# Performance work log

Hardware: AMD Instinct MI355X
Metric: run time of the kernel (lower is better)

## Reference

```python
import jax, jax.numpy as jnp
import numpy as np

B, D_IN, D_GAS, D_LIQ, N_PLATES, D_OUT, N_SWEEPS = 16384, 512, 256, 256, 8, 1000, 2


def _linear_init(key, fan_in, shape):
    bound = 1.0 / np.sqrt(fan_in)
    return jax.random.uniform(key, shape, minval=-bound, maxval=bound, dtype=jnp.float32)


def setup_inputs() -> dict:
    key = jax.random.key(0)
    ks = jax.random.split(key, 13)
    return {
        "x": jax.random.normal(ks[0], (B, D_IN), dtype=jnp.float32),
        # gas encoder: Linear(d_in, d_gas)
        "W_ge": _linear_init(ks[1], D_IN, (D_IN, D_GAS)),
        "b_ge": _linear_init(ks[2], D_IN, (D_GAS,)),
        # shared plate: equilibrium Linear(d_liquid, d_gas)
        "W_eq": _linear_init(ks[3], D_LIQ, (D_LIQ, D_GAS)),
        "b_eq": _linear_init(ks[4], D_LIQ, (D_GAS,)),
        # shared plate: transfer Linear(d_gas, d_gas)
        "W_tr": _linear_init(ks[5], D_GAS, (D_GAS, D_GAS)),
        "b_tr": _linear_init(ks[6], D_GAS, (D_GAS,)),
        # shared plate: absorption Linear(d_gas, d_liquid)
        "W_ab": _linear_init(ks[7], D_GAS, (D_GAS, D_LIQ)),
        "b_ab": _linear_init(ks[8], D_GAS, (D_LIQ,)),
        # transfer coefficient
        "alpha": jnp.float32(0.1),
        # output head: Linear(d_gas+d_liquid, d_gas) -> ReLU -> Linear(d_gas, d_out)
        "W1": _linear_init(ks[9], D_GAS + D_LIQ, (D_GAS + D_LIQ, D_GAS)),
        "b1": _linear_init(ks[10], D_GAS + D_LIQ, (D_GAS,)),
        "W2": _linear_init(ks[11], D_GAS, (D_GAS, D_OUT)),
        "b2": _linear_init(ks[12], D_GAS, (D_OUT,)),
    }


def reference(x, W_ge, b_ge, W_eq, b_eq, W_tr, b_tr, W_ab, b_ab, alpha, W1, b1, W2, b2):
    g0 = jax.nn.relu(x @ W_ge + b_ge)  # (B, d_gas)

    def plate(g, l):
        e = jax.nn.sigmoid(l @ W_eq + b_eq)          # equilibrium gas composition
        df = g - e                                    # driving force
        delta = alpha * (df @ W_tr + b_tr)            # transferred amount
        return g - delta, l + (delta @ W_ab + b_ab)   # gas loses, liquid absorbs

    N = N_PLATES
    g = [g0] + [None] * N
    l = [None] * (N + 1) + [jnp.zeros((x.shape[0], D_LIQ), dtype=x.dtype)]
    for _sweep in range(N_SWEEPS):
        # descending liquid sweep
        for n in range(N, 0, -1):
            g_in = g[n - 1] if g[n - 1] is not None else g0
            _, l[n] = plate(g_in, l[n + 1])
        # ascending gas sweep
        g[0] = g0
        for n in range(1, N + 1):
            g[n], _ = plate(g[n - 1], l[n])

    feats = jnp.concatenate([g[N], l[1]], axis=-1)  # (B, d_gas + d_liquid)
    h = jax.nn.relu(feats @ W1 + b1)
    return h @ W2 + b2
```

## Files before the change

kernel.cpp:

```cpp
#include <hip/hip_runtime.h>


typedef _Float16 f16;
typedef _Float16 f16x8 __attribute__((ext_vector_type(8)));
typedef float f32x4 __attribute__((ext_vector_type(4)));

#define NT 256
#define TILE_B 16
#define SLOT 8192
#define TMPA_OFF 131072
#define TMPB_OFF 139264
#define LDS_BYTES 147456
#define GASP(s) (smem + (s) * SLOT)
#define LIQP(m) (smem + 57344 + (m) * SLOT)

__device__ __forceinline__ f32x4 mfma16(f16x8 a, f16x8 b, f32x4 c) {
  return __builtin_amdgcn_mfma_f32_16x16x32_f16(a, b, c, 0, 0, 0);
}
__device__ __forceinline__ f32x4 zero4() {
  f32x4 z; z[0] = 0.f; z[1] = 0.f; z[2] = 0.f; z[3] = 0.f; return z;
}
__device__ __forceinline__ float sigm(float s) { return 1.f / (1.f + __expf(-s)); }

__device__ __forceinline__ void gemm_rB(const char* aB, const f16x8 (&B)[8][4],
                                        int l15, int kg, f32x4 (&acc)[4]) {
  const int sw = (l15 & 7) << 4;
  #pragma unroll
  for (int ks = 0; ks < 8; ++ks) {
    const int kk = (ks << 5) + (kg << 3);
    f16x8 a = *(const f16x8*)(aB + l15 * 512 + ((kk * 2) ^ sw));
    #pragma unroll
    for (int f = 0; f < 4; ++f) acc[f] = mfma16(a, B[ks][f], acc[f]);
  }
}

template <int K, int AS>
__device__ __forceinline__ void gemm_gB(const char* aB,
                                        const f16* __restrict__ p0,
                                        const f16* __restrict__ p1,
                                        const f16* __restrict__ p2,
                                        const f16* __restrict__ p3,
                                        int l15, int kg, f32x4 (&acc)[4]) {
  const int sw = (l15 & 7) << 4;
  #pragma unroll
  for (int ks = 0; ks < (K >> 5); ++ks) {
    const int kk = (ks << 5) + (kg << 3);
    f16x8 a = *(const f16x8*)(aB + l15 * AS + ((kk * 2) ^ sw));
    acc[0] = mfma16(a, *(const f16x8*)(p0 + (ks << 5)), acc[0]);
    acc[1] = mfma16(a, *(const f16x8*)(p1 + (ks << 5)), acc[1]);
    acc[2] = mfma16(a, *(const f16x8*)(p2 + (ks << 5)), acc[2]);
    acc[3] = mfma16(a, *(const f16x8*)(p3 + (ks << 5)), acc[3]);
  }
}

__device__ __forceinline__ void store16(char* buf, int w, int l15, int kg,
                                        const float* v) {
  #pragma unroll
  for (int q = 0; q < 16; ++q) {
    const int r = kg * 4 + (q & 3);
    const int c = w * 64 + ((q >> 2) << 4) + l15;
    *(f16*)(buf + r * 512 + ((c * 2) ^ ((r & 7) << 4))) = (f16)v[q];
  }
}
__device__ __forceinline__ void read16(const char* buf, int w, int l15, int kg,
                                       float* v) {
  #pragma unroll
  for (int q = 0; q < 16; ++q) {
    const int r = kg * 4 + (q & 3);
    const int c = w * 64 + ((q >> 2) << 4) + l15;
    v[q] = (float)*(const f16*)(buf + r * 512 + ((c * 2) ^ ((r & 7) << 4)));
  }
}

__global__ void prep_all(const float* __restrict__ Wge, const float* __restrict__ Weq,
                         const float* __restrict__ Wtr, const float* __restrict__ Wab,
                         const float* __restrict__ W1,  const float* __restrict__ W2,
                         f16* __restrict__ WgeT, f16* __restrict__ WeqT,
                         f16* __restrict__ WtrT, f16* __restrict__ WabT,
                         f16* __restrict__ W1T,  f16* __restrict__ W2T) {
  __shared__ float ts[32][33];
  const int b = blockIdx.x;
  const float* src; f16* dst; int K, N, Npad, ti;
  if (b < 128)      { src = Wge; dst = WgeT; K = 512; N = 256;  Npad = 256;  ti = b; }
  else if (b < 192) { src = Weq; dst = WeqT; K = 256; N = 256;  Npad = 256;  ti = b - 128; }
  else if (b < 256) { src = Wtr; dst = WtrT; K = 256; N = 256;  Npad = 256;  ti = b - 192; }
  else if (b < 320) { src = Wab; dst = WabT; K = 256; N = 256;  Npad = 256;  ti = b - 256; }
  else if (b < 448) { src = W1;  dst = W1T;  K = 512; N = 256;  Npad = 256;  ti = b - 320; }
  else              { src = W2;  dst = W2T;  K = 256; N = 1000; Npad = 1024; ti = b - 448; }
  const int bnT = Npad >> 5;
  const int bk = (ti / bnT) << 5, bn = (ti % bnT) << 5;
  const int tx = threadIdx.x & 31, ty = threadIdx.x >> 5;
  #pragma unroll
  for (int i = 0; i < 32; i += 8) {
    const int k = bk + ty + i, n = bn + tx;
    ts[ty + i][tx] = (k < K && n < N) ? src[(size_t)k * N + n] : 0.f;
  }
  __syncthreads();
  #pragma unroll
  for (int i = 0; i < 32; i += 8) {
    const int n = bn + ty + i, k = bk + tx;
    if (n < Npad) dst[(size_t)n * K + k] = (f16)ts[tx][ty + i];
  }
}

__global__ __launch_bounds__(NT, 1)
void cfn_main(const float* __restrict__ x,
              const float* __restrict__ bge, const float* __restrict__ beq,
              const float* __restrict__ btr, const float* __restrict__ bab,
              const float* __restrict__ alphap,
              const float* __restrict__ b1p, const float* __restrict__ b2p,
              const f16* __restrict__ WgeT, const f16* __restrict__ WeqT,
              const f16* __restrict__ WtrT, const f16* __restrict__ WabT,
              const f16* __restrict__ W1T, const f16* __restrict__ W2T,
              float* __restrict__ out) {
  extern __shared__ char smem[];
  const int tid = threadIdx.x;
  const int lane = tid & 63;
  const int w = tid >> 6;
  const int l15 = lane & 15, kg = lane >> 4;
  const int r0 = blockIdx.x * TILE_B;
  const float alpha = alphap[0];
  const int sw = (l15 & 7) << 4;

  float beqv[4], btrv[4], babv[4], se[4];
  #pragma unroll
  for (int f = 0; f < 4; ++f) {
    const int c = w * 64 + f * 16 + l15;
    beqv[f] = beq[c]; btrv[f] = btr[c]; babv[f] = bab[c];
    se[f] = sigm(beqv[f]);
  }

  f16x8 WeqR[8][4], WtrR[8][4];
  #pragma unroll
  for (int f = 0; f < 4; ++f) {
    const int c = w * 64 + f * 16 + l15;
    const f16* pe = WeqT + (size_t)c * 256 + kg * 8;
    const f16* pt = WtrT + (size_t)c * 256 + kg * 8;
    #pragma unroll
    for (int ks = 0; ks < 8; ++ks) {
      WeqR[ks][f] = *(const f16x8*)(pe + (ks << 5));
      WtrR[ks][f] = *(const f16x8*)(pt + (ks << 5));
    }
  }

  const f16* wab0 = WabT + (size_t)(w * 64 +  0 + l15) * 256 + kg * 8;
  const f16* wab1 = WabT + (size_t)(w * 64 + 16 + l15) * 256 + kg * 8;
  const f16* wab2 = WabT + (size_t)(w * 64 + 32 + l15) * 256 + kg * 8;
  const f16* wab3 = WabT + (size_t)(w * 64 + 48 + l15) * 256 + kg * 8;

  {
    const int row = tid >> 4;
    const int cb = (tid & 15) << 5;
    const int rs = (row & 7) << 4;
    const float* p = x + (size_t)(r0 + row) * 512 + cb;
    #pragma unroll
    for (int i = 0; i < 4; ++i) {
      float4 u = *(const float4*)(p + i * 8);
      float4 v = *(const float4*)(p + i * 8 + 4);
      f16x8 h;
      h[0] = (f16)u.x; h[1] = (f16)u.y; h[2] = (f16)u.z; h[3] = (f16)u.w;
      h[4] = (f16)v.x; h[5] = (f16)v.y; h[6] = (f16)v.z; h[7] = (f16)v.w;
      *(f16x8*)(smem + row * 1024 + (((cb + i * 8) * 2) ^ rs)) = h;
    }
  }
  __syncthreads();

  {
    f32x4 acc[4] = {zero4(), zero4(), zero4(), zero4()};
    const f16* g0 = WgeT + (size_t)(w * 64 +  0 + l15) * 512 + kg * 8;
    const f16* g1 = WgeT + (size_t)(w * 64 + 16 + l15) * 512 + kg * 8;
    const f16* g2 = WgeT + (size_t)(w * 64 + 32 + l15) * 512 + kg * 8;
    const f16* g3 = WgeT + (size_t)(w * 64 + 48 + l15) * 512 + kg * 8;
    gemm_gB<512, 1024>(smem, g0, g1, g2, g3, l15, kg, acc);
    float G0[16];
    #pragma unroll
    for (int q = 0; q < 16; ++q) {
      const float bv = bge[w * 64 + ((q >> 2) << 4) + l15];
      float v2 = acc[q >> 2][q & 3] + bv;
      G0[q] = v2 > 0.f ? v2 : 0.f;
    }
    __syncthreads();
    #pragma unroll
    for (int s = 0; s < 8; ++s) store16(GASP(s), w, l15, kg, G0);
  }
  __syncthreads();

  float G8[16];

  #pragma unroll 1
  for (int sweep = 0; sweep < 2; ++sweep) {
    #pragma unroll 1
    for (int n = 8; n >= 1; --n) {
      float GV[16];
      read16(GASP(n - 1), w, l15, kg, GV);
      float DF[16];
      if (n == 8) {
        #pragma unroll
        for (int q = 0; q < 16; ++q) DF[q] = GV[q] - se[q >> 2];
      } else {
        f32x4 acc[4] = {zero4(), zero4(), zero4(), zero4()};
        gemm_rB(LIQP(n + 1), WeqR, l15, kg, acc);
        #pragma unroll
        for (int q = 0; q < 16; ++q)
          DF[q] = GV[q] - sigm(acc[q >> 2][q & 3] + beqv[q >> 2]);
      }
      store16(smem + TMPA_OFF, w, l15, kg, DF);
      __syncthreads();
      float DEL[16];
      {
        f32x4 acc[4] = {zero4(), zero4(), zero4(), zero4()};
        gemm_rB(smem + TMPA_OFF, WtrR, l15, kg, acc);
        #pragma unroll
        for (int q = 0; q < 16; ++q)
          DEL[q] = alpha * (acc[q >> 2][q & 3] + btrv[q >> 2]);
      }
      store16(smem + TMPB_OFF, w, l15, kg, DEL);
      __syncthreads();
      {
        f32x4 acc[4] = {zero4(), zero4(), zero4(), zero4()};
        gemm_gB<256, 512>(smem + TMPB_OFF, wab0, wab1, wab2, wab3, l15, kg, acc);
        float LN[16];
        if (n < 8) read16(LIQP(n + 1), w, l15, kg, LN);
        else { _Pragma("unroll") for (int q = 0; q < 16; ++q) LN[q] = 0.f; }
        #pragma unroll
        for (int q = 0; q < 16; ++q)
          LN[q] += acc[q >> 2][q & 3] + babv[q >> 2];
        store16(LIQP(n), w, l15, kg, LN);
      }
      __syncthreads();
    }
    const int nmax = (sweep == 0) ? 7 : 8;
    #pragma unroll 1
    for (int n = 1; n <= nmax; ++n) {
      float GV[16];
      read16(GASP(n - 1), w, l15, kg, GV);
      float DF[16];
      {
        f32x4 acc[4] = {zero4(), zero4(), zero4(), zero4()};
        gemm_rB(LIQP(n), WeqR, l15, kg, acc);
        #pragma unroll
        for (int q = 0; q < 16; ++q)
          DF[q] = GV[q] - sigm(acc[q >> 2][q & 3] + beqv[q >> 2]);
      }
      store16(smem + TMPA_OFF, w, l15, kg, DF);
      __syncthreads();
      {
        f32x4 acc[4] = {zero4(), zero4(), zero4(), zero4()};
        gemm_rB(smem + TMPA_OFF, WtrR, l15, kg, acc);
        if (n < 8) {
          float NG[16];
          #pragma unroll
          for (int q = 0; q < 16; ++q)
            NG[q] = GV[q] - alpha * (acc[q >> 2][q & 3] + btrv[q >> 2]);
          store16(GASP(n), w, l15, kg, NG);
        } else {
          #pragma unroll
          for (int q = 0; q < 16; ++q)
            G8[q] = GV[q] - alpha * (acc[q >> 2][q & 3] + btrv[q >> 2]);
        }
      }
      __syncthreads();
    }
  }

  store16(smem + TMPA_OFF, w, l15, kg, G8);
  __syncthreads();
  {
    f32x4 acc[4] = {zero4(), zero4(), zero4(), zero4()};
    const f16* p0 = W1T + (size_t)(w * 64 +  0 + l15) * 512 + kg * 8;
    const f16* p1 = W1T + (size_t)(w * 64 + 16 + l15) * 512 + kg * 8;
    const f16* p2 = W1T + (size_t)(w * 64 + 32 + l15) * 512 + kg * 8;
    const f16* p3 = W1T + (size_t)(w * 64 + 48 + l15) * 512 + kg * 8;
    #pragma unroll
    for (int ks = 0; ks < 16; ++ks) {
      const int kk = (ks << 5) + (kg << 3);
      const char* base = (ks < 8) ? (smem + TMPA_OFF) : (smem + 65536);
      const int kl = kk & 255;
      f16x8 a = *(const f16x8*)(base + l15 * 512 + ((kl * 2) ^ sw));
      acc[0] = mfma16(a, *(const f16x8*)(p0 + (ks << 5)), acc[0]);
      acc[1] = mfma16(a, *(const f16x8*)(p1 + (ks << 5)), acc[1]);
      acc[2] = mfma16(a, *(const f16x8*)(p2 + (ks << 5)), acc[2]);
      acc[3] = mfma16(a, *(const f16x8*)(p3 + (ks << 5)), acc[3]);
    }
    float H[16];
    #pragma unroll
    for (int q = 0; q < 16; ++q) {
      const float bv = b1p[w * 64 + ((q >> 2) << 4) + l15];
      float v2 = acc[q >> 2][q & 3] + bv;
      H[q] = v2 > 0.f ? v2 : 0.f;
    }
    __syncthreads();
    store16(smem + TMPB_OFF, w, l15, kg, H);
  }
  __syncthreads();

  f32x4 cf[16];
  #pragma unroll
  for (int fi = 0; fi < 16; ++fi) {
    cf[fi] = zero4();
    const int f = w + fi * 4;
    if (f < 63) {
      const f16* p = W2T + (size_t)(f * 16 + l15) * 256 + kg * 8;
      #pragma unroll
      for (int ks = 0; ks < 8; ++ks) {
        const int kk = (ks << 5) + (kg << 3);
        f16x8 a = *(const f16x8*)(smem + TMPB_OFF + l15 * 512 + ((kk * 2) ^ sw));
        cf[fi] = mfma16(a, *(const f16x8*)(p + (ks << 5)), cf[fi]);
      }
    }
  }

  {
    float* ob = (float*)smem;
    #pragma unroll
    for (int fi = 0; fi < 16; ++fi) {
      const int f = w + fi * 4;
      const int colc = f * 16 + l15;
      if (f < 63 && colc < 1000) {
        const float bv = b2p[colc];
        #pragma unroll
        for (int j = 0; j < 4; ++j)
          ob[(kg * 4 + j) * 1000 + colc] = cf[fi][j] + bv;
      }
    }
  }
  __syncthreads();
  {
    const float* ob = (const float*)smem;
    float* op = out + (size_t)r0 * 1000;
    #pragma unroll 1
    for (int i = tid; i < 4000; i += NT)
      *(float4*)(op + i * 4) = *(const float4*)(ob + i * 4);
  }
}

extern "C" void kernel_launch(void* const* d_in, const int* in_sizes, int n_in,
                              void* d_out, int out_size, void* d_ws, size_t ws_size,
                              hipStream_t stream) {
  const float* x   = (const float*)d_in[0];
  const float* Wge = (const float*)d_in[1];
  const float* bge = (const float*)d_in[2];
  const float* Weq = (const float*)d_in[3];
  const float* beq = (const float*)d_in[4];
  const float* Wtr = (const float*)d_in[5];
  const float* btr = (const float*)d_in[6];
  const float* Wab = (const float*)d_in[7];
  const float* bab = (const float*)d_in[8];
  const float* alp = (const float*)d_in[9];
  const float* W1  = (const float*)d_in[10];
  const float* b1  = (const float*)d_in[11];
  const float* W2  = (const float*)d_in[12];
  const float* b2  = (const float*)d_in[13];
  float* out = (float*)d_out;

  char* ws = (char*)d_ws;
  f16* WgeT = (f16*)(ws + 0);
  f16* WeqT = (f16*)(ws + 262144);
  f16* WtrT = (f16*)(ws + 393216);
  f16* WabT = (f16*)(ws + 524288);
  f16* W1T  = (f16*)(ws + 655360);
  f16* W2T  = (f16*)(ws + 917504);

  prep_all<<<704, 256, 0, stream>>>(Wge, Weq, Wtr, Wab, W1, W2,
                                    WgeT, WeqT, WtrT, WabT, W1T, W2T);

  (void)hipFuncSetAttribute(reinterpret_cast<const void*>(cfn_main),
                            hipFuncAttributeMaxDynamicSharedMemorySize, LDS_BYTES);
  cfn_main<<<16384 / TILE_B, NT, LDS_BYTES, stream>>>(
      x, bge, beq, btr, bab, alp, b1, b2,
      WgeT, WeqT, WtrT, WabT, W1T, W2T, out);
}
```

Measured before the change: 799.3 us.

## Fold transfer and absorption weights into one matrix, keep gas states in registers

Precomputes Wtab = alpha*Wtr@Wab and a matching fused bias, so the descending liquid sweep does two GEMMs per plate instead of three and one fewer LDS round trip and barrier. Gas plate states move from LDS slots into fp16 register arrays accessed through switch statements. The Weq and Wtr register caches are dropped in favour of reading B operands from global/L2. Together these cut LDS from 144KB to 80KB and allow two blocks per CU. The cost is extra global weight traffic per GEMM, slightly different fp16 rounding from the pre-multiplied matrix, and register pressure under the tighter launch bound.

```diff
diff --git a/kernel.cpp b/kernel.cpp
--- a/kernel.cpp
+++ b/kernel.cpp
@@ -2,17 +2,17 @@
 
 
 typedef _Float16 f16;
+typedef _Float16 f16x2 __attribute__((ext_vector_type(2)));
 typedef _Float16 f16x8 __attribute__((ext_vector_type(8)));
 typedef float f32x4 __attribute__((ext_vector_type(4)));
 
 #define NT 256
 #define TILE_B 16
 #define SLOT 8192
-#define TMPA_OFF 131072
-#define TMPB_OFF 139264
-#define LDS_BYTES 147456
-#define GASP(s) (smem + (s) * SLOT)
-#define LIQP(m) (smem + 57344 + (m) * SLOT)
+#define TMPA_OFF 65536
+#define TMPH_OFF 73728
+#define LDS_BYTES 81920
+#define LIQP(m) (smem + ((m) - 1) * SLOT)
 
 __device__ __forceinline__ f32x4 mfma16(f16x8 a, f16x8 b, f32x4 c) {
   return __builtin_amdgcn_mfma_f32_16x16x32_f16(a, b, c, 0, 0, 0);
@@ -21,18 +21,6 @@
   f32x4 z; z[0] = 0.f; z[1] = 0.f; z[2] = 0.f; z[3] = 0.f; return z;
 }
 __device__ __forceinline__ float sigm(float s) { return 1.f / (1.f + __expf(-s)); }
-
-__device__ __forceinline__ void gemm_rB(const char* aB, const f16x8 (&B)[8][4],
-                                        int l15, int kg, f32x4 (&acc)[4]) {
-  const int sw = (l15 & 7) << 4;
-  #pragma unroll
-  for (int ks = 0; ks < 8; ++ks) {
-    const int kk = (ks << 5) + (kg << 3);
-    f16x8 a = *(const f16x8*)(aB + l15 * 512 + ((kk * 2) ^ sw));
-    #pragma unroll
-    for (int f = 0; f < 4; ++f) acc[f] = mfma16(a, B[ks][f], acc[f]);
-  }
-}
 
 template <int K, int AS>
 __device__ __forceinline__ void gemm_gB(const char* aB,
@@ -62,31 +50,38 @@
     *(f16*)(buf + r * 512 + ((c * 2) ^ ((r & 7) << 4))) = (f16)v[q];
   }
 }
-__device__ __forceinline__ void read16(const char* buf, int w, int l15, int kg,
-                                       float* v) {
-  #pragma unroll
-  for (int q = 0; q < 16; ++q) {
-    const int r = kg * 4 + (q & 3);
-    const int c = w * 64 + ((q >> 2) << 4) + l15;
-    v[q] = (float)*(const f16*)(buf + r * 512 + ((c * 2) ^ ((r & 7) << 4)));
+
+#define GH_RD(S) { _Pragma("unroll") for (int q = 0; q < 16; ++q) v[q] = (float)gh[S][q >> 1][q & 1]; }
+__device__ __forceinline__ void gh_read(const f16x2 (&gh)[8][8], int s, float* v) {
+  switch (s) {
+    case 0: GH_RD(0) break; case 1: GH_RD(1) break; case 2: GH_RD(2) break;
+    case 3: GH_RD(3) break; case 4: GH_RD(4) break; case 5: GH_RD(5) break;
+    case 6: GH_RD(6) break; default: GH_RD(7) break;
+  }
+}
+#define GH_WR(S) { _Pragma("unroll") for (int q = 0; q < 16; ++q) gh[S][q >> 1][q & 1] = (f16)v[q]; }
+__device__ __forceinline__ void gh_write(f16x2 (&gh)[8][8], int s, const float* v) {
+  switch (s) {
+    case 1: GH_WR(1) break; case 2: GH_WR(2) break; case 3: GH_WR(3) break;
+    case 4: GH_WR(4) break; case 5: GH_WR(5) break; case 6: GH_WR(6) break;
+    default: GH_WR(7) break;
   }
 }
 
 __global__ void prep_all(const float* __restrict__ Wge, const float* __restrict__ Weq,
-                         const float* __restrict__ Wtr, const float* __restrict__ Wab,
-                         const float* __restrict__ W1,  const float* __restrict__ W2,
+                         const float* __restrict__ Wtr, const float* __restrict__ W1,
+                         const float* __restrict__ W2,
                          f16* __restrict__ WgeT, f16* __restrict__ WeqT,
-                         f16* __restrict__ WtrT, f16* __restrict__ WabT,
-                         f16* __restrict__ W1T,  f16* __restrict__ W2T) {
+                         f16* __restrict__ WtrT, f16* __restrict__ W1T,
+                         f16* __restrict__ W2T) {
   __shared__ float ts[32][33];
   const int b = blockIdx.x;
   const float* src; f16* dst; int K, N, Npad, ti;
   if (b < 128)      { src = Wge; dst = WgeT; K = 512; N = 256;  Npad = 256;  ti = b; }
   else if (b < 192) { src = Weq; dst = WeqT; K = 256; N = 256;  Npad = 256;  ti = b - 128; }
   else if (b < 256) { src = Wtr; dst = WtrT; K = 256; N = 256;  Npad = 256;  ti = b - 192; }
-  else if (b < 320) { src = Wab; dst = WabT; K = 256; N = 256;  Npad = 256;  ti = b - 256; }
-  else if (b < 448) { src = W1;  dst = W1T;  K = 512; N = 256;  Npad = 256;  ti = b - 320; }
-  else              { src = W2;  dst = W2T;  K = 256; N = 1000; Npad = 1024; ti = b - 448; }
+  else if (b < 384) { src = W1;  dst = W1T;  K = 512; N = 256;  Npad = 256;  ti = b - 256; }
+  else              { src = W2;  dst = W2T;  K = 256; N = 1000; Npad = 1024; ti = b - 384; }
   const int bnT = Npad >> 5;
   const int bk = (ti / bnT) << 5, bn = (ti % bnT) << 5;
   const int tx = threadIdx.x & 31, ty = threadIdx.x >> 5;
@@ -103,14 +98,39 @@
   }
 }
 
-__global__ __launch_bounds__(NT, 1)
+__global__ void prep_wtab(const float* __restrict__ Wtr, const float* __restrict__ Wab,
+                          const float* __restrict__ btr, const float* __restrict__ bab,
+                          const float* __restrict__ alphap,
+                          f16* __restrict__ WtabT, float* __restrict__ btab) {
+  __shared__ float wcol[256];
+  __shared__ float pr[256];
+  const int out = blockIdx.x;
+  const int k = threadIdx.x;
+  wcol[k] = Wab[(size_t)k * 256 + out];
+  pr[k] = btr[k] * Wab[(size_t)k * 256 + out];
+  __syncthreads();
+  float acc = 0.f;
+  const float* wr = Wtr + (size_t)k * 256;
+  #pragma unroll 4
+  for (int m = 0; m < 256; ++m) acc += wr[m] * wcol[m];
+  const float alpha = alphap[0];
+  WtabT[(size_t)out * 256 + k] = (f16)(alpha * acc);
+  if (k == 0) {
+    float s = 0.f;
+    for (int m = 0; m < 256; ++m) s += pr[m];
+    btab[out] = alpha * s + bab[out];
+  }
+}
+
+__global__ __launch_bounds__(NT, 2)
 void cfn_main(const float* __restrict__ x,
               const float* __restrict__ bge, const float* __restrict__ beq,
-              const float* __restrict__ btr, const float* __restrict__ bab,
+              const float* __restrict__ btr,
               const float* __restrict__ alphap,
               const float* __restrict__ b1p, const float* __restrict__ b2p,
               const f16* __restrict__ WgeT, const f16* __restrict__ WeqT,
-              const f16* __restrict__ WtrT, const f16* __restrict__ WabT,
+              const f16* __restrict__ WtrT, const f16* __restrict__ WtabT,
+              const float* __restrict__ btab,
               const f16* __restrict__ W1T, const f16* __restrict__ W2T,
               float* __restrict__ out) {
   extern __shared__ char smem[];
@@ -122,31 +142,26 @@
   const float alpha = alphap[0];
   const int sw = (l15 & 7) << 4;
 
-  float beqv[4], btrv[4], babv[4], se[4];
+  float beqv[4], btrv[4], btabv[4], se[4];
   #pragma unroll
   for (int f = 0; f < 4; ++f) {
     const int c = w * 64 + f * 16 + l15;
-    beqv[f] = beq[c]; btrv[f] = btr[c]; babv[f] = bab[c];
+    beqv[f] = beq[c]; btrv[f] = btr[c]; btabv[f] = btab[c];
     se[f] = sigm(beqv[f]);
   }
 
-  f16x8 WeqR[8][4], WtrR[8][4];
-  #pragma unroll
-  for (int f = 0; f < 4; ++f) {
-    const int c = w * 64 + f * 16 + l15;
-    const f16* pe = WeqT + (size_t)c * 256 + kg * 8;
-    const f16* pt = WtrT + (size_t)c * 256 + kg * 8;
-    #pragma unroll
-    for (int ks = 0; ks < 8; ++ks) {
-      WeqR[ks][f] = *(const f16x8*)(pe + (ks << 5));
-      WtrR[ks][f] = *(const f16x8*)(pt + (ks << 5));
-    }
-  }
-
-  const f16* wab0 = WabT + (size_t)(w * 64 +  0 + l15) * 256 + kg * 8;
-  const f16* wab1 = WabT + (size_t)(w * 64 + 16 + l15) * 256 + kg * 8;
-  const f16* wab2 = WabT + (size_t)(w * 64 + 32 + l15) * 256 + kg * 8;
-  const f16* wab3 = WabT + (size_t)(w * 64 + 48 + l15) * 256 + kg * 8;
+  const f16* weq0  = WeqT  + (size_t)(w * 64 +  0 + l15) * 256 + kg * 8;
+  const f16* weq1  = WeqT  + (size_t)(w * 64 + 16 + l15) * 256 + kg * 8;
+  const f16* weq2  = WeqT  + (size_t)(w * 64 + 32 + l15) * 256 + kg * 8;
+  const f16* weq3  = WeqT  + (size_t)(w * 64 + 48 + l15) * 256 + kg * 8;
+  const f16* wtr0  = WtrT  + (size_t)(w * 64 +  0 + l15) * 256 + kg * 8;
+  const f16* wtr1  = WtrT  + (size_t)(w * 64 + 16 + l15) * 256 + kg * 8;
+  const f16* wtr2  = WtrT  + (size_t)(w * 64 + 32 + l15) * 256 + kg * 8;
+  const f16* wtr3  = WtrT  + (size_t)(w * 64 + 48 + l15) * 256 + kg * 8;
+  const f16* wtab0 = WtabT + (size_t)(w * 64 +  0 + l15) * 256 + kg * 8;
+  const f16* wtab1 = WtabT + (size_t)(w * 64 + 16 + l15) * 256 + kg * 8;
+  const f16* wtab2 = WtabT + (size_t)(w * 64 + 32 + l15) * 256 + kg * 8;
+  const f16* wtab3 = WtabT + (size_t)(w * 64 + 48 + l15) * 256 + kg * 8;
 
   {
     const int row = tid >> 4;
@@ -165,6 +180,7 @@
   }
   __syncthreads();
 
+  f16x2 gh[8][8];
   {
     f32x4 acc[4] = {zero4(), zero4(), zero4(), zero4()};
     const f16* g0 = WgeT + (size_t)(w * 64 +  0 + l15) * 512 + kg * 8;
@@ -172,92 +188,82 @@
     const f16* g2 = WgeT + (size_t)(w * 64 + 32 + l15) * 512 + kg * 8;
     const f16* g3 = WgeT + (size_t)(w * 64 + 48 + l15) * 512 + kg * 8;
     gemm_gB<512, 1024>(smem, g0, g1, g2, g3, l15, kg, acc);
-    float G0[16];
     #pragma unroll
     for (int q = 0; q < 16; ++q) {
       const float bv = bge[w * 64 + ((q >> 2) << 4) + l15];
       float v2 = acc[q >> 2][q & 3] + bv;
-      G0[q] = v2 > 0.f ? v2 : 0.f;
-    }
-    __syncthreads();
-    #pragma unroll
-    for (int s = 0; s < 8; ++s) store16(GASP(s), w, l15, kg, G0);
+      v2 = v2 > 0.f ? v2 : 0.f;
+      const f16 hv = (f16)v2;
+      #pragma unroll
+      for (int s = 0; s < 8; ++s) gh[s][q >> 1][q & 1] = hv;
+    }
   }
   __syncthreads();
 
   float G8[16];
+  #pragma unroll
+  for (int q = 0; q < 16; ++q) G8[q] = 0.f;
 
   #pragma unroll 1
   for (int sweep = 0; sweep < 2; ++sweep) {
     #pragma unroll 1
     for (int n = 8; n >= 1; --n) {
-      float GV[16];
-      read16(GASP(n - 1), w, l15, kg, GV);
+      float v[16];
+      gh_read(gh, n - 1, v);
       float DF[16];
       if (n == 8) {
         #pragma unroll
-        for (int q = 0; q < 16; ++q) DF[q] = GV[q] - se[q >> 2];
+        for (int q = 0; q < 16; ++q) DF[q] = v[q] - se[q >> 2];
       } else {
         f32x4 acc[4] = {zero4(), zero4(), zero4(), zero4()};
-        gemm_rB(LIQP(n + 1), WeqR, l15, kg, acc);
+        gemm_gB<256, 512>(LIQP(n + 1), weq0, weq1, weq2, weq3, l15, kg, acc);
         #pragma unroll
         for (int q = 0; q < 16; ++q)
-          DF[q] = GV[q] - sigm(acc[q >> 2][q & 3] + beqv[q >> 2]);
-      }
-      store16(smem + TMPA_OFF, w, l15, kg, DF);
-      __syncthreads();
-      float DEL[16];
-      {
-        f32x4 acc[4] = {zero4(), zero4(), zero4(), zero4()};
-        gemm_rB(smem + TMPA_OFF, WtrR, l15, kg, acc);
-        #pragma unroll
-        for (int q = 0; q < 16; ++q)
-          DEL[q] = alpha * (acc[q >> 2][q & 3] + btrv[q >> 2]);
-      }
-      store16(smem + TMPB_OFF, w, l15, kg, DEL);
-      __syncthreads();
-      {
-        f32x4 acc[4] = {zero4(), zero4(), zero4(), zero4()};
-        gemm_gB<256, 512>(smem + TMPB_OFF, wab0, wab1, wab2, wab3, l15, kg, acc);
-        float LN[16];
-        if (n < 8) read16(LIQP(n + 1), w, l15, kg, LN);
-        else { _Pragma("unroll") for (int q = 0; q < 16; ++q) LN[q] = 0.f; }
-        #pragma unroll
-        for (int q = 0; q < 16; ++q)
-          LN[q] += acc[q >> 2][q & 3] + babv[q >> 2];
-        store16(LIQP(n), w, l15, kg, LN);
-      }
-      __syncthreads();
-    }
-    const int nmax = (sweep == 0) ? 7 : 8;
-    #pragma unroll 1
-    for (int n = 1; n <= nmax; ++n) {
-      float GV[16];
-      read16(GASP(n - 1), w, l15, kg, GV);
-      float DF[16];
-      {
-        f32x4 acc[4] = {zero4(), zero4(), zero4(), zero4()};
-        gemm_rB(LIQP(n), WeqR, l15, kg, acc);
-        #pragma unroll
-        for (int q = 0; q < 16; ++q)
-          DF[q] = GV[q] - sigm(acc[q >> 2][q & 3] + beqv[q >> 2]);
+          DF[q] = v[q] - sigm(acc[q >> 2][q & 3] + beqv[q >> 2]);
       }
       store16(smem + TMPA_OFF, w, l15, kg, DF);
       __syncthreads();
       {
         f32x4 acc[4] = {zero4(), zero4(), zero4(), zero4()};
-        gemm_rB(smem + TMPA_OFF, WtrR, l15, kg, acc);
-        if (n < 8) {
-          float NG[16];
-          #pragma unroll
-          for (int q = 0; q < 16; ++q)
-            NG[q] = GV[q] - alpha * (acc[q >> 2][q & 3] + btrv[q >> 2]);
-          store16(GASP(n), w, l15, kg, NG);
-        } else {
-          #pragma unroll
-          for (int q = 0; q < 16; ++q)
-            G8[q] = GV[q] - alpha * (acc[q >> 2][q & 3] + btrv[q >> 2]);
+        gemm_gB<256, 512>(smem + TMPA_OFF, wtab0, wtab1, wtab2, wtab3, l15, kg, acc);
+        char* dst = LIQP(n);
+        const char* prv = LIQP(n + 1);
+        #pragma unroll
+        for (int q = 0; q < 16; ++q) {
+          const int r = kg * 4 + (q & 3);
+          const int c = w * 64 + ((q >> 2) << 4) + l15;
+          const int off = r * 512 + ((c * 2) ^ ((r & 7) << 4));
+          float lp = 0.f;
+          if (n < 8) lp = (float)*(const f16*)(prv + off);
+          *(f16*)(dst + off) = (f16)(lp + acc[q >> 2][q & 3] + btabv[q >> 2]);
         }
+      }
+      __syncthreads();
+    }
+    const int nmax = (sweep == 0) ? 7 : 8;
+    #pragma unroll 1
+    for (int n = 1; n <= nmax; ++n) {
+      float v[16];
+      gh_read(gh, n - 1, v);
+      float DF[16];
+      {
+        f32x4 acc[4] = {zero4(), zero4(), zero4(), zero4()};
+        gemm_gB<256, 512>(LIQP(n), weq0, weq1, weq2, weq3, l15, kg, acc);
+        #pragma unroll
+        for (int q = 0; q < 16; ++q)
+          DF[q] = v[q] - sigm(acc[q >> 2][q & 3] + beqv[q >> 2]);
+      }
+      store16(smem + TMPA_OFF, w, l15, kg, DF);
+      __syncthreads();
+      {
+        f32x4 acc[4] = {zero4(), zero4(), zero4(), zero4()};
+        gemm_gB<256, 512>(smem + TMPA_OFF, wtr0, wtr1, wtr2, wtr3, l15, kg, acc);
+        float ng[16];
+        #pragma unroll
+        for (int q = 0; q < 16; ++q)
+          ng[q] = v[q] - alpha * (acc[q >> 2][q & 3] + btrv[q >> 2]);
+        if (n < 8) gh_write(gh, n, ng);
+        else { _Pragma("unroll") for (int q = 0; q < 16; ++q) G8[q] = ng[q]; }
       }
       __syncthreads();
     }
@@ -274,7 +280,7 @@
     #pragma unroll
     for (int ks = 0; ks < 16; ++ks) {
       const int kk = (ks << 5) + (kg << 3);
-      const char* base = (ks < 8) ? (smem + TMPA_OFF) : (smem + 65536);
+      const char* base = (ks < 8) ? (smem + TMPA_OFF) : LIQP(1);
       const int kl = kk & 255;
       f16x8 a = *(const f16x8*)(base + l15 * 512 + ((kl * 2) ^ sw));
       acc[0] = mfma16(a, *(const f16x8*)(p0 + (ks << 5)), acc[0]);
@@ -289,8 +295,7 @@
       float v2 = acc[q >> 2][q & 3] + bv;
       H[q] = v2 > 0.f ? v2 : 0.f;
     }
-    __syncthreads();
-    store16(smem + TMPB_OFF, w, l15, kg, H);
+    store16(smem + TMPH_OFF, w, l15, kg, H);
   }
   __syncthreads();
 
@@ -304,11 +309,12 @@
       #pragma unroll
       for (int ks = 0; ks < 8; ++ks) {
         const int kk = (ks << 5) + (kg << 3);
-        f16x8 a = *(const f16x8*)(smem + TMPB_OFF + l15 * 512 + ((kk * 2) ^ sw));
+        f16x8 a = *(const f16x8*)(smem + TMPH_OFF + l15 * 512 + ((kk * 2) ^ sw));
         cf[fi] = mfma16(a, *(const f16x8*)(p + (ks << 5)), cf[fi]);
       }
     }
   }
+  __syncthreads();
 
   {
     float* ob = (float*)smem;
@@ -354,19 +360,21 @@
   float* out = (float*)d_out;
 
   char* ws = (char*)d_ws;
-  f16* WgeT = (f16*)(ws + 0);
-  f16* WeqT = (f16*)(ws + 262144);
-  f16* WtrT = (f16*)(ws + 393216);
-  f16* WabT = (f16*)(ws + 524288);
-  f16* W1T  = (f16*)(ws + 655360);
-  f16* W2T  = (f16*)(ws + 917504);
-
-  prep_all<<<704, 256, 0, stream>>>(Wge, Weq, Wtr, Wab, W1, W2,
-                                    WgeT, WeqT, WtrT, WabT, W1T, W2T);
+  f16* WgeT  = (f16*)(ws + 0);
+  f16* WeqT  = (f16*)(ws + 262144);
+  f16* WtrT  = (f16*)(ws + 393216);
+  f16* W1T   = (f16*)(ws + 524288);
+  f16* W2T   = (f16*)(ws + 786432);
+  f16* WtabT = (f16*)(ws + 1310720);
+  float* btabp = (float*)(ws + 1441792);
+
+  prep_all<<<640, 256, 0, stream>>>(Wge, Weq, Wtr, W1, W2,
+                                    WgeT, WeqT, WtrT, W1T, W2T);
+  prep_wtab<<<256, 256, 0, stream>>>(Wtr, Wab, btr, bab, alp, WtabT, btabp);
 
   (void)hipFuncSetAttribute(reinterpret_cast<const void*>(cfn_main),
                             hipFuncAttributeMaxDynamicSharedMemorySize, LDS_BYTES);
   cfn_main<<<16384 / TILE_B, NT, LDS_BYTES, stream>>>(
-      x, bge, beq, btr, bab, alp, b1, b2,
-      WgeT, WeqT, WtrT, WabT, W1T, W2T, out);
-}
+      x, bge, beq, btr, alp, b1, b2,
+      WgeT, WeqT, WtrT, WtabT, btabp, W1T, W2T, out);
+}
```

New measurement: 1.570 ms. 96.4% more time.
